# Performance work log

Measured on AMD Instinct MI355X. Metric: run time of the kernel, lower is better.

The kernel has to match this reference:

```python
import math
import jax, jax.numpy as jnp
import numpy as np
from jax.scipy.special import erf

BATCH, SEQ, DIM = 2, 4096, 128
EMA_HEADS, DQK, DV = 16, 64, 256
NUM_BUCKETS, MAX_DIST = 32, 128


def _next_fast_len(n):
    # smallest 5-smooth integer >= n (matches scipy.fftpack.next_fast_len)
    while True:
        m = n
        for p in (2, 3, 5):
            while m % p == 0:
                m //= p
        if m == 1:
            return n
        n += 1


def _laplacian_attn(x):
    mu = math.sqrt(0.5)
    std = math.sqrt(0.25 * math.pi)
    return 0.5 * (1.0 + erf((x - mu) / (std * math.sqrt(2.0))))


def _rel_pos_bias(table, n, scale):
    # causal T5 relative position bias, bucket(q_pos - k_pos)
    pos = jnp.arange(n)
    rel = jnp.maximum(pos[:, None] - pos[None, :], 0)  # [n, n], >= 0
    max_exact = NUM_BUCKETS // 2
    is_small = rel < max_exact
    val_large = max_exact + (
        jnp.log(jnp.maximum(rel, 1).astype(jnp.float32) / max_exact)
        / math.log(MAX_DIST / max_exact) * (NUM_BUCKETS - max_exact)
    ).astype(jnp.int32)
    val_large = jnp.minimum(val_large, NUM_BUCKETS - 1)
    bucket = jnp.where(is_small, rel, val_large)
    return table[bucket, 0] * scale  # [n, n]


def _conv1d_fft(x, K, n):
    # x: [b, n, h, d] (fft over axis 1), K: [n, h] (fft over axis 0)
    fast_len = _next_fast_len(2 * n - 1)
    f_x = jnp.fft.rfft(x, n=fast_len, axis=1)
    f_K = jnp.fft.rfft(K, n=fast_len, axis=0)
    out = jnp.fft.irfft(f_x * jnp.conj(f_K)[None, :, :, None], fast_len, axis=1)
    out = jnp.roll(out, -1, axis=1)
    return out[:, fast_len - n:]  # [b, n, h, d]


def _forward(x, expansion, reduction, alphas, dampen, Wqk, bqk, gamma, beta,
             Wv, bv, rel_table, Wr, br, Wu, bu, Wh, Uh, bh):
    b, n, d = x.shape
    # ---- multi-headed EMA (causal -> unidirectional) via FFT conv ----
    xe = jnp.einsum('bnd,hd->bnhd', x, expansion)
    a = jax.nn.sigmoid(alphas)            # [h]
    dm = jax.nn.sigmoid(dampen)           # [h]
    powers = jnp.arange(n - 1, -1, -1, dtype=x.dtype)  # reversed powers
    K = a * ((1.0 - a) * dm) ** powers[:, None]        # [n, h]
    conv = _conv1d_fft(xe, K, n)
    ema = jnp.einsum('bnhd,hd->bnd', conv, reduction)  # [b, n, d]
    # ---- single-headed attention (chunk_size=-1 -> one chunk), v from x ----
    qk = jax.nn.silu(ema @ Wqk + bqk)     # [b, n, dqk]
    q = qk * gamma[0] + beta[0]
    k = qk * gamma[1] + beta[1]
    v = jax.nn.silu(x @ Wv + bv)          # [b, n, dv]
    scale = 1.0 / n                       # laplacian_attn_fn scaling
    sim = jnp.einsum('bid,bjd->bij', q, k) * scale
    sim = sim + _rel_pos_bias(rel_table, n, DQK ** 0.5)
    attn = _laplacian_attn(sim)
    causal_mask = jnp.triu(jnp.ones((n, n), dtype=bool), 1)
    attn = jnp.where(causal_mask, 0.0, attn)  # laplacian: zero after activation
    attn_out = jnp.einsum('bij,bjd->bid', attn, v)  # [b, n, dv]
    # ---- gating + output ----
    reset_gate = jax.nn.silu(ema @ Wr + br)         # [b, n, dv]
    update_gate = jax.nn.sigmoid(ema @ Wu + bu)     # [b, n, d]
    gated = attn_out * reset_gate
    H = jax.nn.silu(ema @ Wh + gated @ Uh + bh)     # [b, n, d]
    return update_gate * H + (1.0 - update_gate) * x


def setup_inputs() -> dict:
    key = jax.random.key(0)
    ks = jax.random.split(key, 18)
    def rn(i, shape, s=1.0):
        return jax.random.normal(ks[i], shape, dtype=jnp.float32) * s
    return dict(
        x=rn(0, (BATCH, SEQ, DIM)),
        expansion=rn(1, (EMA_HEADS, DIM), 0.2),
        reduction=rn(2, (EMA_HEADS, DIM), 0.2),
        alphas=rn(3, (EMA_HEADS,)),
        dampen=rn(4, (EMA_HEADS,)),
        Wqk=rn(5, (DIM, DQK), 0.05), bqk=rn(6, (DQK,), 0.02),
        gamma=rn(7, (2, DQK), 0.02), beta=jnp.zeros((2, DQK), jnp.float32),
        Wv=rn(8, (DIM, DV), 0.05), bv=rn(9, (DV,), 0.02),
        rel_table=rn(10, (NUM_BUCKETS, 1), 0.02),
        Wr=rn(11, (DIM, DV), 0.05), br=rn(12, (DV,), 0.02),
        Wu=rn(13, (DIM, DIM), 0.05), bu=rn(14, (DIM,), 0.02),
        Wh=rn(15, (DIM, DIM), 0.05), Uh=rn(16, (DV, DIM), 0.05),
        bh=rn(17, (DIM,), 0.02),
    )


def reference(x, expansion, reduction, alphas, dampen, Wqk, bqk, gamma, beta,
              Wv, bv, rel_table, Wr, br, Wu, bu, Wh, Uh, bh):
    return _forward(x, expansion, reduction, alphas, dampen, Wqk, bqk, gamma,
                    beta, Wv, bv, rel_table, Wr, br, Wu, bu, Wh, Uh, bh)
```

## Files before the change

kernel.cpp:

```cpp
#include <hip/hip_runtime.h>
#include <cstdint>
#include <cmath>

#define B_ 2
#define N_ 4096
#define D_ 128
#define H_ 16
#define DQK_ 64
#define DV_ 256

typedef float    f4_t  __attribute__((ext_vector_type(4)));
typedef float    f16f  __attribute__((ext_vector_type(16)));
typedef _Float16 h4_t  __attribute__((ext_vector_type(4)));
typedef _Float16 h8_t  __attribute__((ext_vector_type(8)));

__device__ __forceinline__ float sigmoidf_(float z) { return 1.f/(1.f + expf(-z)); }
__device__ __forceinline__ float siluf_(float z)    { return z/(1.f + expf(-z)); }
__device__ __forceinline__ f16f zero16() {
  f16f z;
#pragma unroll
  for (int i = 0; i < 16; ++i) z[i] = 0.f;
  return z;
}

__global__ void ema_phase1(const float* __restrict__ x, const float* __restrict__ expansion,
                           const float* __restrict__ alphas, const float* __restrict__ dampen,
                           float* __restrict__ F, _Float16* __restrict__ xh) {
  int bid = blockIdx.x;
  int dg = bid & 7, c = (bid >> 3) & 63, b = bid >> 9;
  int h = threadIdx.x & 15, dl = threadIdx.x >> 4;
  int d = dg*16 + dl;
  float a  = sigmoidf_(alphas[h]);
  float dm = sigmoidf_(dampen[h]);
  float q  = (1.f - a)*dm;
  float coef = a * expansion[h*D_ + d];
  __shared__ float xs[64][16];
  {
    int e = threadIdx.x;
    int t = e >> 2, seg = e & 3;
    const float* xp = x + ((size_t)b*N_ + c*64 + t)*D_ + dg*16 + seg*4;
    f4_t v = *(const f4_t*)xp;
    *(f4_t*)&xs[t][seg*4] = v;
    h4_t hv;
#pragma unroll
    for (int j = 0; j < 4; ++j) hv[j] = (_Float16)v[j];
    *(h4_t*)(xh + ((size_t)b*N_ + c*64 + t)*D_ + dg*16 + seg*4) = hv;
  }
  __syncthreads();
  float s = 0.f;
#pragma unroll
  for (int t = 0; t < 64; ++t) s = fmaf(q, s, coef*xs[t][dl]);
  F[(((size_t)b*H_ + h)*D_ + d)*64 + c] = s;
}

__global__ void ema_carry(const float* __restrict__ F, const float* __restrict__ alphas,
                          const float* __restrict__ dampen, float* __restrict__ carry) {
  int wid = blockIdx.x*4 + (threadIdx.x >> 6);
  int lane = threadIdx.x & 63;
  int h = (wid >> 7) & 15;
  float a  = sigmoidf_(alphas[h]);
  float dm = sigmoidf_(dampen[h]);
  float q  = (1.f - a)*dm;
  float qL = q;
#pragma unroll
  for (int i = 0; i < 6; ++i) qL *= qL;
  float A = qL;
  float Bv = F[(size_t)wid*64 + lane];
#pragma unroll
  for (int len = 1; len < 64; len <<= 1) {
    float Ap = __shfl_up(A, len);
    float Bp = __shfl_up(Bv, len);
    if (lane >= len) { Bv = fmaf(A, Bp, Bv); A = A*Ap; }
  }
  float Bprev = __shfl_up(Bv, 1);
  carry[(size_t)wid*64 + lane] = (lane == 0) ? 0.f : Bprev;
}

__global__ void ema_phase2(const float* __restrict__ x, const float* __restrict__ expansion,
                           const float* __restrict__ reduction,
                           const float* __restrict__ alphas, const float* __restrict__ dampen,
                           const float* __restrict__ carry, _Float16* __restrict__ emah) {
  int bid = blockIdx.x;
  int dg = bid & 7, c = (bid >> 3) & 63, b = bid >> 9;
  int h = threadIdx.x & 15, dl = threadIdx.x >> 4;
  int d = dg*16 + dl;
  float a  = sigmoidf_(alphas[h]);
  float dm = sigmoidf_(dampen[h]);
  float q  = (1.f - a)*dm;
  float coef = a * expansion[h*D_ + d];
  float red  = reduction[h*D_ + d];
  __shared__ float xs[64][16];
  {
    int e = threadIdx.x;
    int t = e >> 2, seg = e & 3;
    const float* xp = x + ((size_t)b*N_ + c*64 + t)*D_ + dg*16 + seg*4;
    *(f4_t*)&xs[t][seg*4] = *(const f4_t*)xp;
  }
  __syncthreads();
  float s = carry[(((size_t)b*H_ + h)*D_ + d)*64 + c];
  for (int t = 0; t < 64; ++t) {
    s = fmaf(q, s, coef*xs[t][dl]);
    float v = red * s;
    v += __shfl_xor(v, 1); v += __shfl_xor(v, 2);
    v += __shfl_xor(v, 4); v += __shfl_xor(v, 8);
    if (h == 0) emah[((size_t)b*N_ + c*64 + t)*D_ + d] = (_Float16)v;
  }
}

__global__ void prep_all(const float* __restrict__ Wqk, const float* __restrict__ Wv,
                         const float* __restrict__ Wr, const float* __restrict__ Wu,
                         const float* __restrict__ Wh,
                         const float* __restrict__ bqk, const float* __restrict__ bv,
                         const float* __restrict__ br, const float* __restrict__ bu,
                         const float* __restrict__ bh,
                         const float* __restrict__ Uh, const float* __restrict__ rel_table,
                         _Float16* __restrict__ Wt, float* __restrict__ bcat,
                         _Float16* __restrict__ Uht, float* __restrict__ bias2T) {
  int idx = blockIdx.x*256 + threadIdx.x;
  if (idx < 832*128) {
    int c = idx >> 7, d = idx & 127;
    const float* W; const float* bias; int ncol, cl;
    if (c < 64)       { W=Wqk; bias=bqk; ncol=64;  cl=c; }
    else if (c < 320) { W=Wv;  bias=bv;  ncol=256; cl=c-64; }
    else if (c < 576) { W=Wr;  bias=br;  ncol=256; cl=c-320; }
    else if (c < 704) { W=Wu;  bias=bu;  ncol=128; cl=c-576; }
    else              { W=Wh;  bias=bh;  ncol=128; cl=c-704; }
    Wt[idx] = (_Float16)W[d*ncol + cl];
    if (d == 0) bcat[c] = bias[cl];
  } else if (idx < 832*128 + 32768) {
    int i2 = idx - 832*128;
    int k = i2 >> 7, c = i2 & 127;
    Uht[(size_t)c*256 + k] = (_Float16)Uh[i2];
  } else if (idx < 832*128 + 32768 + 4096) {
    int r = idx - (832*128 + 32768);
    int bucket;
    if (r < 16) bucket = r;
    else {
      double v = log((double)r / 16.0) / log(8.0) * 16.0;
      bucket = 16 + (int)v;
      if (bucket > 31) bucket = 31;
    }
    bias2T[r] = (rel_table[bucket]*8.0f - 0.70710678f) * 1.1283792f;
  }
}

__global__ __launch_bounds__(256) void linear_mfma(
    const _Float16* __restrict__ emah, const _Float16* __restrict__ xh,
    const _Float16* __restrict__ Wt, const float* __restrict__ bcat,
    const float* __restrict__ gamma, const float* __restrict__ beta,
    _Float16* __restrict__ qh, _Float16* __restrict__ kh, _Float16* __restrict__ vTt,
    _Float16* __restrict__ resetbh, _Float16* __restrict__ updatebh,
    float* __restrict__ hemab) {
  int slab = blockIdx.x % 13, rt = blockIdx.x / 13;
  int tid = threadIdx.x;
  int lane = tid & 63, w = tid >> 6;
  int lr = lane & 15, lg = lane >> 4;
  int mode = (slab==0)?0:(slab<5)?1:(slab<9)?2:(slab<11)?3:4;
  const _Float16* src = (mode==1) ? xh : emah;
  __shared__ _Float16 As[64][136];
  __shared__ _Float16 Ws[64][136];
  {
    const h8_t* s8 = (const h8_t*)(src + (size_t)rt*64*D_);
#pragma unroll
    for (int i = 0; i < 4; ++i) {
      int idx = tid + i*256;
      int row = idx >> 4, seg = idx & 15;
      *(h8_t*)&As[row][seg*8] = s8[idx];
    }
    const h8_t* w8 = (const h8_t*)(Wt + (size_t)slab*64*D_);
#pragma unroll
    for (int i = 0; i < 4; ++i) {
      int idx = tid + i*256;
      int row = idx >> 4, seg = idx & 15;
      *(h8_t*)&Ws[row][seg*8] = w8[idx];
    }
  }
  __syncthreads();
  h4_t af[8];
#pragma unroll
  for (int ks = 0; ks < 8; ++ks) af[ks] = *(const h4_t*)&As[w*16 + lr][ks*16 + lg*4];
  int row0 = rt*64 + w*16 + lg*4;
#pragma unroll
  for (int ns = 0; ns < 4; ++ns) {
    f4_t acc = (f4_t){0.f,0.f,0.f,0.f};
#pragma unroll
    for (int ks = 0; ks < 8; ++ks) {
      h4_t bf = *(const h4_t*)&Ws[ns*16 + lr][ks*16 + lg*4];
      acc = __builtin_amdgcn_mfma_f32_16x16x16f16(af[ks], bf, acc, 0, 0, 0);
    }
    int c = slab*64 + ns*16 + lr;
    float bias = bcat[c];
    if (mode == 0) {
      float g0 = gamma[c], g1 = gamma[64+c], be0 = beta[c], be1 = beta[64+c];
#pragma unroll
      for (int r = 0; r < 4; ++r) {
        float qk = siluf_(acc[r] + bias);
        size_t row = row0 + r;
        qh[row*DQK_ + c] = (_Float16)(qk*g0 + be0);
        kh[row*DQK_ + c] = (_Float16)(qk*g1 + be1);
      }
    } else if (mode == 1) {
      int cl = c - 64;
      int bb = row0 >> 12, rl = row0 & 4095;
      h4_t vv;
#pragma unroll
      for (int r = 0; r < 4; ++r) vv[r] = (_Float16)siluf_(acc[r] + bias);
      *(h4_t*)&vTt[(((size_t)bb*128 + (rl>>5))*256 + cl)*32 + (rl&31)] = vv;
    } else if (mode == 2) {
      int cl = c - 320;
#pragma unroll
      for (int r = 0; r < 4; ++r)
        resetbh[(size_t)(row0 + r)*DV_ + cl] = (_Float16)siluf_(acc[r] + bias);
    } else if (mode == 3) {
      int cl = c - 576;
#pragma unroll
      for (int r = 0; r < 4; ++r)
        updatebh[(size_t)(row0 + r)*D_ + cl] = (_Float16)sigmoidf_(acc[r] + bias);
    } else {
      int cl = c - 704;
#pragma unroll
      for (int r = 0; r < 4; ++r) hemab[(size_t)(row0 + r)*D_ + cl] = acc[r] + bias;
    }
  }
}

__global__ __launch_bounds__(512, 2) void attn_kernel(
    const _Float16* __restrict__ qh, const _Float16* __restrict__ kh,
    const _Float16* __restrict__ vTt, const float* __restrict__ bias2T,
    _Float16* __restrict__ attnp) {
  int bid = blockIdx.x;
  int ip = 31 - (bid >> 5);
  int rem = bid & 31;
  int s = rem >> 1, b = rem & 1;
  int nblk = (ip + 2) >> 1;
  if (s >= nblk) return;
  int T = 4*ip + 4;
  int tlo = (s*T)/nblk, thi = ((s+1)*T)/nblk;
  int nt = thi - tlo;
  int tq = ip >> 1;
  int base = (ip & 1) ? (tq+1)*(tq+1) : tq*(tq+1);
  int slot = base + s;
  int i0 = ip*128;
  int tid = threadIdx.x;
  int lane = tid & 63, w = tid >> 6;
  int iq = w & 3;
  int dvh = w >> 2;
  bool prod = (dvh == 0);
  int lm = lane & 31, lg = lane >> 5;

  __shared__ __align__(16) char Vb[2][18432];
  __shared__ __align__(16) char Kb[2][4352];
  __shared__ __align__(16) char Pb[2][4][2560];
  __shared__ float biasW[384];

  int jmaxv = thi*32 - 1;
  int dlo = i0 - jmaxv;
  int cnt = 128 + jmaxv - tlo*32;
  for (int k = tid; k < cnt; k += 512) {
    int d = dlo + k;
    biasW[k] = d < 0 ? -1e38f : bias2T[d];
  }

  h4_t qf[8];
  if (prod) {
    const _Float16* qp = qh + ((size_t)b*N_ + i0 + iq*32 + lm)*DQK_ + 4*lg;
#pragma unroll
    for (int ksq = 0; ksq < 8; ++ksq) qf[ksq] = *(const h4_t*)(qp + 8*ksq);
  }

  f16f accO[4];
#pragma unroll
  for (int i = 0; i < 4; ++i) accO[i] = zero16();

  const _Float16* kbase = kh + (size_t)b*N_*DQK_;
  const _Float16* vbase = vTt + (size_t)b*128*8192;
  int st = tid & 255;
  int kr = st >> 3, kc = st & 7;

  h8_t k8r, vr4[4];
#define ISSUE_(JT) { \
  k8r = *(const h8_t*)(kbase + (size_t)((JT)*32 + kr)*DQK_ + kc*8); \
  const _Float16* vp_ = vbase + (size_t)(JT)*8192 + st*32; \
  _Pragma("unroll") for (int i = 0; i < 4; ++i) vr4[i] = *(const h8_t*)(vp_ + i*8); }

#define COMMIT_(BI) { \
  char* ka_ = Kb[BI] + kr*136 + kc*16; \
  *(h4_t*)ka_       = __builtin_shufflevector(k8r, k8r, 0,1,2,3); \
  *(h4_t*)(ka_ + 8) = __builtin_shufflevector(k8r, k8r, 4,5,6,7); \
  char* va_ = Vb[BI] + st*72; \
  _Pragma("unroll") for (int i = 0; i < 4; ++i) { \
    *(h4_t*)(va_ + i*16)     = __builtin_shufflevector(vr4[i], vr4[i], 0,1,2,3); \
    *(h4_t*)(va_ + i*16 + 8) = __builtin_shufflevector(vr4[i], vr4[i], 4,5,6,7); } }

  if (!prod) {
    ISSUE_(tlo);
    COMMIT_(0);
    if (nt > 1) ISSUE_(tlo + 1);
  }
  __syncthreads();

  const float C1 = 1.1283792f / 4096.f;
  int ibase = i0 + iq*32 + lm;
#pragma unroll 1
  for (int t = 0; t < nt; ++t) {
    h4_t pa[4];
    if (prod) {
      const char* kb = Kb[t & 1];
      __builtin_amdgcn_s_setprio(1);
      f16f accS = zero16();
#pragma unroll
      for (int ksq = 0; ksq < 8; ++ksq) {
        h4_t kf = *(const h4_t*)(kb + lm*136 + 16*ksq + 8*lg);
        accS = __builtin_amdgcn_mfma_f32_32x32x8f16(kf, qf[ksq], accS, 0, 0, 0);
      }
      __builtin_amdgcn_s_setprio(0);
      int idx0 = ibase - dlo - (tlo + t)*32 - 4*lg;
#pragma unroll
      for (int rr = 0; rr < 16; ++rr) {
        float tt = fmaf(accS[rr], C1, biasW[idx0 - 8*(rr>>2) - (rr&3)]);
        float e = tt*fmaf(tt*tt, -0.101797f, -2.304877f);
        float u = exp2f(e);
        float pv = __builtin_amdgcn_rcpf(1.f + u);
        pa[rr>>2][rr&3] = (_Float16)pv;
      }
      char* pp = Pb[t & 1][iq] + lane*40;
#pragma unroll
      for (int k2 = 0; k2 < 4; ++k2) *(h4_t*)(pp + k2*8) = pa[k2];
    } else {
      if (t+1 < nt) COMMIT_((t+1) & 1);
      if (t+2 < nt) ISSUE_(tlo + t + 2);
    }
    __syncthreads();
    if (!prod) {
      const char* pp = Pb[t & 1][iq] + lane*40;
#pragma unroll
      for (int k2 = 0; k2 < 4; ++k2) pa[k2] = *(const h4_t*)(pp + k2*8);
    }
    const char* vb = Vb[t & 1];
    __builtin_amdgcn_s_setprio(1);
#pragma unroll
    for (int ks = 0; ks < 4; ++ks) {
#pragma unroll
      for (int dvb = 0; dvb < 4; ++dvb) {
        h4_t vf = *(const h4_t*)(vb + (dvh*128 + dvb*32 + lm)*72 + 16*ks + 8*lg);
        accO[dvb] = __builtin_amdgcn_mfma_f32_32x32x8f16(pa[ks], vf, accO[dvb], 0, 0, 0);
      }
    }
    __builtin_amdgcn_s_setprio(0);
    __syncthreads();
  }
#undef ISSUE_
#undef COMMIT_

  _Float16* op = attnp + ((size_t)b*272 + slot)*(128*256);
#pragma unroll
  for (int dvb = 0; dvb < 4; ++dvb) {
    int col = dvh*128 + dvb*32 + lm;
#pragma unroll
    for (int rr = 0; rr < 16; ++rr) {
      int row = iq*32 + 8*(rr>>2) + 4*lg + (rr&3);
      op[(size_t)row*256 + col] = (_Float16)accO[dvb][rr];
    }
  }
}

__global__ void combine_gated(const _Float16* __restrict__ attnp,
                              const _Float16* __restrict__ resetbh,
                              _Float16* __restrict__ gatedh) {
  size_t fi = (size_t)blockIdx.x*256 + threadIdx.x;
  int c4 = (int)(fi & 63);
  int rr = (int)(fi >> 6);
  int b = rr >> 12, n = rr & 4095;
  int ip = n >> 7, rowLocal = n & 127;
  int nblk = (ip + 2) >> 1;
  int tq = ip >> 1;
  int base = (ip & 1) ? (tq+1)*(tq+1) : tq*(tq+1);
  const _Float16* ap = attnp + ((size_t)b*272 + base)*32768 + (size_t)rowLocal*256 + c4*4;
  f4_t acc = (f4_t){0.f,0.f,0.f,0.f};
  for (int s2 = 0; s2 < nblk; ++s2) {
    h4_t pv = *(const h4_t*)(ap + (size_t)s2*32768);
#pragma unroll
    for (int j = 0; j < 4; ++j) acc[j] += (float)pv[j];
  }
  h4_t rg = *(const h4_t*)(resetbh + fi*4);
  h4_t hg;
#pragma unroll
  for (int j = 0; j < 4; ++j) hg[j] = (_Float16)(acc[j] * (float)rg[j]);
  *(h4_t*)(gatedh + fi*4) = hg;
}

__global__ __launch_bounds__(256) void final_mfma(
    const _Float16* __restrict__ gatedh, const _Float16* __restrict__ Uht,
    const float* __restrict__ hemab, const _Float16* __restrict__ updatebh,
    const float* __restrict__ x, float* __restrict__ out) {
  int rt = blockIdx.x >> 1, cs = blockIdx.x & 1;
  int tid = threadIdx.x;
  int lane = tid & 63, w = tid >> 6;
  int lr = lane & 15, lg = lane >> 4;
  int row0 = rt*64, c0 = cs*64;
  __shared__ _Float16 As[64][136];
  __shared__ _Float16 Ws[64][136];
  f4_t acc[4];
#pragma unroll
  for (int ns = 0; ns < 4; ++ns) acc[ns] = (f4_t){0.f,0.f,0.f,0.f};
#pragma unroll
  for (int kc = 0; kc < 2; ++kc) {
    __syncthreads();
#pragma unroll
    for (int i = 0; i < 4; ++i) {
      int idx = tid + i*256;
      int row = idx >> 4, seg = idx & 15;
      *(h8_t*)&As[row][seg*8] =
          *(const h8_t*)(gatedh + (size_t)(row0 + row)*DV_ + kc*128 + seg*8);
      *(h8_t*)&Ws[row][seg*8] =
          *(const h8_t*)(Uht + (size_t)(c0 + row)*DV_ + kc*128 + seg*8);
    }
    __syncthreads();
    h4_t af[8];
#pragma unroll
    for (int ks = 0; ks < 8; ++ks) af[ks] = *(const h4_t*)&As[w*16 + lr][ks*16 + lg*4];
#pragma unroll
    for (int ns = 0; ns < 4; ++ns) {
#pragma unroll
      for (int ks = 0; ks < 8; ++ks) {
        h4_t bf = *(const h4_t*)&Ws[ns*16 + lr][ks*16 + lg*4];
        acc[ns] = __builtin_amdgcn_mfma_f32_16x16x16f16(af[ks], bf, acc[ns], 0, 0, 0);
      }
    }
  }
  int orow = row0 + w*16 + lg*4;
#pragma unroll
  for (int ns = 0; ns < 4; ++ns) {
    int col = c0 + ns*16 + lr;
#pragma unroll
    for (int r = 0; r < 4; ++r) {
      size_t o = (size_t)(orow + r)*D_ + col;
      float z = acc[ns][r] + hemab[o];
      float Hv = siluf_(z);
      float u  = (float)updatebh[o];
      out[o] = u*Hv + (1.f - u)*x[o];
    }
  }
}

extern "C" void kernel_launch(void* const* d_in, const int* in_sizes, int n_in,
                              void* d_out, int out_size, void* d_ws, size_t ws_size,
                              hipStream_t stream) {
  (void)in_sizes; (void)n_in; (void)out_size; (void)ws_size;
  const float* x         = (const float*)d_in[0];
  const float* expansion = (const float*)d_in[1];
  const float* reduction = (const float*)d_in[2];
  const float* alphas    = (const float*)d_in[3];
  const float* dampen    = (const float*)d_in[4];
  const float* Wqk       = (const float*)d_in[5];
  const float* bqk       = (const float*)d_in[6];
  const float* gamma     = (const float*)d_in[7];
  const float* beta      = (const float*)d_in[8];
  const float* Wv        = (const float*)d_in[9];
  const float* bv        = (const float*)d_in[10];
  const float* rel_table = (const float*)d_in[11];
  const float* Wr        = (const float*)d_in[12];
  const float* br        = (const float*)d_in[13];
  const float* Wu        = (const float*)d_in[14];
  const float* bu        = (const float*)d_in[15];
  const float* Wh        = (const float*)d_in[16];
  const float* Uh        = (const float*)d_in[17];
  const float* bh        = (const float*)d_in[18];
  float* out = (float*)d_out;

  char* p = (char*)d_ws;
  size_t off = 0;
  auto alloc = [&](size_t bytes) -> char* {
    char* r = p + off;
    off += (bytes + 255) & ~(size_t)255;
    return r;
  };
  float*    F       = (float*)alloc((size_t)B_*H_*D_*64*4);
  float*    carry   = (float*)alloc((size_t)B_*H_*D_*64*4);
  _Float16* emah    = (_Float16*)alloc((size_t)B_*N_*D_*2);
  _Float16* xh      = (_Float16*)alloc((size_t)B_*N_*D_*2);
  float*    bias2T  = (float*)alloc((size_t)N_*4);
  _Float16* Wt      = (_Float16*)alloc((size_t)832*128*2);
  float*    bcat    = (float*)alloc((size_t)832*4);
  _Float16* Uht     = (_Float16*)alloc((size_t)D_*DV_*2);
  _Float16* qh      = (_Float16*)alloc((size_t)B_*N_*DQK_*2);
  _Float16* kh      = (_Float16*)alloc((size_t)B_*N_*DQK_*2);
  _Float16* vTt     = (_Float16*)alloc((size_t)B_*DV_*N_*2);
  _Float16* resetbh = (_Float16*)alloc((size_t)B_*N_*DV_*2);
  _Float16* updatebh= (_Float16*)alloc((size_t)B_*N_*D_*2);
  float*    hemab   = (float*)alloc((size_t)B_*N_*D_*4);
  _Float16* gatedh  = (_Float16*)alloc((size_t)B_*N_*DV_*2);
  _Float16* attnp   = (_Float16*)alloc((size_t)B_*272*128*256*2);

  prep_all<<<560, 256, 0, stream>>>(Wqk, Wv, Wr, Wu, Wh, bqk, bv, br, bu, bh,
                                    Uh, rel_table, Wt, bcat, Uht, bias2T);
  ema_phase1<<<1024, 256, 0, stream>>>(x, expansion, alphas, dampen, F, xh);
  ema_carry<<<1024, 256, 0, stream>>>(F, alphas, dampen, carry);
  ema_phase2<<<1024, 256, 0, stream>>>(x, expansion, reduction, alphas, dampen, carry, emah);
  linear_mfma<<<128*13, 256, 0, stream>>>(emah, xh, Wt, bcat, gamma, beta,
                                          qh, kh, vTt, resetbh, updatebh, hemab);
  attn_kernel<<<1024, 512, 0, stream>>>(qh, kh, vTt, bias2T, attnp);
  combine_gated<<<2048, 256, 0, stream>>>(attnp, resetbh, gatedh);
  final_mfma<<<256, 256, 0, stream>>>(gatedh, Uht, hemab, updatebh, x, out);
}
```

Baseline: 122.5 us.

## Halve attention query tile, load K into registers, and software-pipeline QK ahead of PV

```diff
diff --git a/kernel.cpp b/kernel.cpp
--- a/kernel.cpp
+++ b/kernel.cpp
@@ -224,115 +224,134 @@
   }
 }
 
-__global__ __launch_bounds__(512, 2) void attn_kernel(
+__global__ __launch_bounds__(256, 3) void attn_kernel(
     const _Float16* __restrict__ qh, const _Float16* __restrict__ kh,
     const _Float16* __restrict__ vTt, const float* __restrict__ bias2T,
     _Float16* __restrict__ attnp) {
   int bid = blockIdx.x;
-  int ip = 31 - (bid >> 5);
+  int it = 63 - (bid >> 5);
   int rem = bid & 31;
   int s = rem >> 1, b = rem & 1;
-  int nblk = (ip + 2) >> 1;
+  int a = it >> 2, r = it & 3;
+  int nblk = a + 1;
   if (s >= nblk) return;
-  int T = 4*ip + 4;
+  int T = 2*it + 2;
   int tlo = (s*T)/nblk, thi = ((s+1)*T)/nblk;
   int nt = thi - tlo;
-  int tq = ip >> 1;
-  int base = (ip & 1) ? (tq+1)*(tq+1) : tq*(tq+1);
+  int base = it + 2*a*(a-1) + r*a;
   int slot = base + s;
-  int i0 = ip*128;
+  int i0 = it * 64;
   int tid = threadIdx.x;
   int lane = tid & 63, w = tid >> 6;
-  int iq = w & 3;
-  int dvh = w >> 2;
+  int ih = w & 1;
+  int dvh = w >> 1;
   bool prod = (dvh == 0);
   int lm = lane & 31, lg = lane >> 5;
 
   __shared__ __align__(16) char Vb[2][18432];
-  __shared__ __align__(16) char Kb[2][4352];
-  __shared__ __align__(16) char Pb[2][4][2560];
-  __shared__ float biasW[384];
+  __shared__ __align__(16) char Pb[2][2][2560];
+  __shared__ float biasW[320];
 
   int jmaxv = thi*32 - 1;
   int dlo = i0 - jmaxv;
-  int cnt = 128 + jmaxv - tlo*32;
-  for (int k = tid; k < cnt; k += 512) {
+  int cnt = 64 + jmaxv - tlo*32;
+  for (int k = tid; k < cnt; k += 256) {
     int d = dlo + k;
     biasW[k] = d < 0 ? -1e38f : bias2T[d];
   }
 
-  h4_t qf[8];
-  if (prod) {
-    const _Float16* qp = qh + ((size_t)b*N_ + i0 + iq*32 + lm)*DQK_ + 4*lg;
-#pragma unroll
-    for (int ksq = 0; ksq < 8; ++ksq) qf[ksq] = *(const h4_t*)(qp + 8*ksq);
-  }
-
-  f16f accO[4];
-#pragma unroll
-  for (int i = 0; i < 4; ++i) accO[i] = zero16();
-
   const _Float16* kbase = kh + (size_t)b*N_*DQK_;
   const _Float16* vbase = vTt + (size_t)b*128*8192;
-  int st = tid & 255;
-  int kr = st >> 3, kc = st & 7;
-
-  h8_t k8r, vr4[4];
-#define ISSUE_(JT) { \
-  k8r = *(const h8_t*)(kbase + (size_t)((JT)*32 + kr)*DQK_ + kc*8); \
-  const _Float16* vp_ = vbase + (size_t)(JT)*8192 + st*32; \
-  _Pragma("unroll") for (int i = 0; i < 4; ++i) vr4[i] = *(const h8_t*)(vp_ + i*8); }
-
-#define COMMIT_(BI) { \
-  char* ka_ = Kb[BI] + kr*136 + kc*16; \
-  *(h4_t*)ka_       = __builtin_shufflevector(k8r, k8r, 0,1,2,3); \
-  *(h4_t*)(ka_ + 8) = __builtin_shufflevector(k8r, k8r, 4,5,6,7); \
-  char* va_ = Vb[BI] + st*72; \
+
+  h4_t qf[8], knxt[8];
+  if (prod) {
+    const _Float16* qp = qh + ((size_t)b*N_ + i0 + ih*32 + lm)*DQK_ + 4*lg;
+#pragma unroll
+    for (int ksq = 0; ksq < 8; ++ksq) qf[ksq] = *(const h4_t*)(qp + 8*ksq);
+  }
+
+#define KISSUE_(JT) { \
+  const _Float16* kp_ = kbase + (size_t)((JT)*32 + lm)*DQK_ + 4*lg; \
+  _Pragma("unroll") for (int ksq = 0; ksq < 8; ++ksq) knxt[ksq] = *(const h4_t*)(kp_ + 8*ksq); }
+
+  f16f accO[4];
+#pragma unroll
+  for (int i = 0; i < 4; ++i) accO[i] = zero16();
+
+  int st = tid & 127;
+  h8_t vr[8];
+#define VISSUE_(JT) { \
+  const _Float16* vp_ = vbase + (size_t)(JT)*8192 + st*64; \
+  _Pragma("unroll") for (int i = 0; i < 8; ++i) vr[i] = *(const h8_t*)(vp_ + i*8); }
+
+#define VCOMMIT_(BI) { \
+  char* va_ = Vb[BI] + (2*st)*72; \
   _Pragma("unroll") for (int i = 0; i < 4; ++i) { \
-    *(h4_t*)(va_ + i*16)     = __builtin_shufflevector(vr4[i], vr4[i], 0,1,2,3); \
-    *(h4_t*)(va_ + i*16 + 8) = __builtin_shufflevector(vr4[i], vr4[i], 4,5,6,7); } }
+    *(h4_t*)(va_ + i*16)     = __builtin_shufflevector(vr[i], vr[i], 0,1,2,3); \
+    *(h4_t*)(va_ + i*16 + 8) = __builtin_shufflevector(vr[i], vr[i], 4,5,6,7); } \
+  char* vb2_ = Vb[BI] + (2*st + 1)*72; \
+  _Pragma("unroll") for (int i = 0; i < 4; ++i) { \
+    *(h4_t*)(vb2_ + i*16)     = __builtin_shufflevector(vr[4+i], vr[4+i], 0,1,2,3); \
+    *(h4_t*)(vb2_ + i*16 + 8) = __builtin_shufflevector(vr[4+i], vr[4+i], 4,5,6,7); } }
+
+  const float C1 = 1.1283792f / 4096.f;
+  int ibase = i0 + ih*32 + lm;
+
+#define SOFTMAX_(JT, ACC, PA) { \
+  int idx0 = ibase - dlo - (JT)*32 - 4*lg; \
+  _Pragma("unroll") for (int rr = 0; rr < 16; ++rr) { \
+    float tt = fmaf((ACC)[rr], C1, biasW[idx0 - 8*(rr>>2) - (rr&3)]); \
+    float e = tt*fmaf(tt*tt, -0.101797f, -2.304877f); \
+    float u = exp2f(e); \
+    float pv = __builtin_amdgcn_rcpf(1.f + u); \
+    (PA)[rr>>2][rr&3] = (_Float16)pv; } }
 
   if (!prod) {
-    ISSUE_(tlo);
-    COMMIT_(0);
-    if (nt > 1) ISSUE_(tlo + 1);
+    VISSUE_(tlo);
+    VCOMMIT_(0);
+    if (nt > 1) VISSUE_(tlo + 1);
+  } else {
+    KISSUE_(tlo);
   }
   __syncthreads();
 
-  const float C1 = 1.1283792f / 4096.f;
-  int ibase = i0 + iq*32 + lm;
+  h4_t paP[4];
+  if (prod) {
+    f16f accS = zero16();
+#pragma unroll
+    for (int ksq = 0; ksq < 8; ++ksq)
+      accS = __builtin_amdgcn_mfma_f32_32x32x8f16(knxt[ksq], qf[ksq], accS, 0, 0, 0);
+    if (nt > 1) KISSUE_(tlo + 1);
+    SOFTMAX_(tlo, accS, paP);
+    char* pp = Pb[0][ih] + lane*40;
+#pragma unroll
+    for (int k2 = 0; k2 < 4; ++k2) *(h4_t*)(pp + k2*8) = paP[k2];
+  }
+  __syncthreads();
+
 #pragma unroll 1
   for (int t = 0; t < nt; ++t) {
-    h4_t pa[4];
+    h4_t pa[4], pan[4];
     if (prod) {
-      const char* kb = Kb[t & 1];
-      __builtin_amdgcn_s_setprio(1);
-      f16f accS = zero16();
-#pragma unroll
-      for (int ksq = 0; ksq < 8; ++ksq) {
-        h4_t kf = *(const h4_t*)(kb + lm*136 + 16*ksq + 8*lg);
-        accS = __builtin_amdgcn_mfma_f32_32x32x8f16(kf, qf[ksq], accS, 0, 0, 0);
+      if (t+1 < nt) {
+        __builtin_amdgcn_s_setprio(1);
+        f16f accS = zero16();
+#pragma unroll
+        for (int ksq = 0; ksq < 8; ++ksq)
+          accS = __builtin_amdgcn_mfma_f32_32x32x8f16(knxt[ksq], qf[ksq], accS, 0, 0, 0);
+        __builtin_amdgcn_s_setprio(0);
+        if (t+2 < nt) KISSUE_(tlo + t + 2);
+        SOFTMAX_(tlo + t + 1, accS, pan);
+        char* pp = Pb[(t+1) & 1][ih] + lane*40;
+#pragma unroll
+        for (int k2 = 0; k2 < 4; ++k2) *(h4_t*)(pp + k2*8) = pan[k2];
       }
-      __builtin_amdgcn_s_setprio(0);
-      int idx0 = ibase - dlo - (tlo + t)*32 - 4*lg;
-#pragma unroll
-      for (int rr = 0; rr < 16; ++rr) {
-        float tt = fmaf(accS[rr], C1, biasW[idx0 - 8*(rr>>2) - (rr&3)]);
-        float e = tt*fmaf(tt*tt, -0.101797f, -2.304877f);
-        float u = exp2f(e);
-        float pv = __builtin_amdgcn_rcpf(1.f + u);
-        pa[rr>>2][rr&3] = (_Float16)pv;
-      }
-      char* pp = Pb[t & 1][iq] + lane*40;
-#pragma unroll
-      for (int k2 = 0; k2 < 4; ++k2) *(h4_t*)(pp + k2*8) = pa[k2];
+#pragma unroll
+      for (int k2 = 0; k2 < 4; ++k2) pa[k2] = paP[k2];
     } else {
-      if (t+1 < nt) COMMIT_((t+1) & 1);
-      if (t+2 < nt) ISSUE_(tlo + t + 2);
-    }
-    __syncthreads();
-    if (!prod) {
-      const char* pp = Pb[t & 1][iq] + lane*40;
+      if (t+1 < nt) VCOMMIT_((t+1) & 1);
+      if (t+2 < nt) VISSUE_(tlo + t + 2);
+      const char* pp = Pb[t & 1][ih] + lane*40;
 #pragma unroll
       for (int k2 = 0; k2 < 4; ++k2) pa[k2] = *(const h4_t*)(pp + k2*8);
     }
@@ -348,17 +367,23 @@
     }
     __builtin_amdgcn_s_setprio(0);
     __syncthreads();
-  }
-#undef ISSUE_
-#undef COMMIT_
-
-  _Float16* op = attnp + ((size_t)b*272 + slot)*(128*256);
+    if (prod) {
+#pragma unroll
+      for (int k2 = 0; k2 < 4; ++k2) paP[k2] = pan[k2];
+    }
+  }
+#undef KISSUE_
+#undef VISSUE_
+#undef VCOMMIT_
+#undef SOFTMAX_
+
+  _Float16* op = attnp + ((size_t)b*544 + slot)*(64*256);
 #pragma unroll
   for (int dvb = 0; dvb < 4; ++dvb) {
     int col = dvh*128 + dvb*32 + lm;
 #pragma unroll
     for (int rr = 0; rr < 16; ++rr) {
-      int row = iq*32 + 8*(rr>>2) + 4*lg + (rr&3);
+      int row = ih*32 + 8*(rr>>2) + 4*lg + (rr&3);
       op[(size_t)row*256 + col] = (_Float16)accO[dvb][rr];
     }
   }
@@ -371,14 +396,14 @@
   int c4 = (int)(fi & 63);
   int rr = (int)(fi >> 6);
   int b = rr >> 12, n = rr & 4095;
-  int ip = n >> 7, rowLocal = n & 127;
-  int nblk = (ip + 2) >> 1;
-  int tq = ip >> 1;
-  int base = (ip & 1) ? (tq+1)*(tq+1) : tq*(tq+1);
-  const _Float16* ap = attnp + ((size_t)b*272 + base)*32768 + (size_t)rowLocal*256 + c4*4;
+  int it = n >> 6, rowLocal = n & 63;
+  int a = it >> 2, r = it & 3;
+  int nblk = a + 1;
+  int base = it + 2*a*(a-1) + r*a;
+  const _Float16* ap = attnp + ((size_t)b*544 + base)*16384 + rowLocal*256 + c4*4;
   f4_t acc = (f4_t){0.f,0.f,0.f,0.f};
   for (int s2 = 0; s2 < nblk; ++s2) {
-    h4_t pv = *(const h4_t*)(ap + (size_t)s2*32768);
+    h4_t pv = *(const h4_t*)(ap + (size_t)s2*16384);
 #pragma unroll
     for (int j = 0; j < 4; ++j) acc[j] += (float)pv[j];
   }
@@ -490,7 +515,7 @@
   _Float16* updatebh= (_Float16*)alloc((size_t)B_*N_*D_*2);
   float*    hemab   = (float*)alloc((size_t)B_*N_*D_*4);
   _Float16* gatedh  = (_Float16*)alloc((size_t)B_*N_*DV_*2);
-  _Float16* attnp   = (_Float16*)alloc((size_t)B_*272*128*256*2);
+  _Float16* attnp   = (_Float16*)alloc((size_t)B_*544*64*256*2);
 
   prep_all<<<560, 256, 0, stream>>>(Wqk, Wv, Wr, Wu, Wh, bqk, bv, br, bu, bh,
                                     Uh, rel_table, Wt, bcat, Uht, bias2T);
@@ -499,7 +524,7 @@
   ema_phase2<<<1024, 256, 0, stream>>>(x, expansion, reduction, alphas, dampen, carry, emah);
   linear_mfma<<<128*13, 256, 0, stream>>>(emah, xh, Wt, bcat, gamma, beta,
                                           qh, kh, vTt, resetbh, updatebh, hemab);
-  attn_kernel<<<1024, 512, 0, stream>>>(qh, kh, vTt, bias2T, attnp);
+  attn_kernel<<<2048, 256, 0, stream>>>(qh, kh, vTt, bias2T, attnp);
   combine_gated<<<2048, 256, 0, stream>>>(attnp, resetbh, gatedh);
   final_mfma<<<256, 256, 0, stream>>>(gatedh, Uht, hemab, updatebh, x, out);
 }
```

Result: slower. 167.4 us (+36.7%).

## Restructure attention to independent per-wave 32-row tiles without shared memory

Applied to the files above, without the earlier changes.

```diff
diff --git a/kernel.cpp b/kernel.cpp
--- a/kernel.cpp
+++ b/kernel.cpp
@@ -224,141 +224,99 @@
   }
 }
 
-__global__ __launch_bounds__(512, 2) void attn_kernel(
+__global__ __launch_bounds__(256, 2) void attn_kernel(
     const _Float16* __restrict__ qh, const _Float16* __restrict__ kh,
     const _Float16* __restrict__ vTt, const float* __restrict__ bias2T,
     _Float16* __restrict__ attnp) {
   int bid = blockIdx.x;
-  int ip = 31 - (bid >> 5);
-  int rem = bid & 31;
-  int s = rem >> 1, b = rem & 1;
-  int nblk = (ip + 2) >> 1;
+  int i32 = 127 - (bid >> 3);
+  int rem = bid & 7;
+  int b = rem & 1, sg = rem >> 1;
+  int w = threadIdx.x >> 6, lane = threadIdx.x & 63;
+  int s = sg*4 + w;
+  int nblk = (i32 >> 3) + 1;
   if (s >= nblk) return;
-  int T = 4*ip + 4;
+  int T = i32 + 1;
   int tlo = (s*T)/nblk, thi = ((s+1)*T)/nblk;
   int nt = thi - tlo;
-  int tq = ip >> 1;
-  int base = (ip & 1) ? (tq+1)*(tq+1) : tq*(tq+1);
+  int t8 = i32 >> 3, r8 = i32 & 7;
+  int base = i32 + 4*t8*(t8-1) + r8*t8;
   int slot = base + s;
-  int i0 = ip*128;
-  int tid = threadIdx.x;
-  int lane = tid & 63, w = tid >> 6;
-  int iq = w & 3;
-  int dvh = w >> 2;
-  bool prod = (dvh == 0);
+  int i0 = i32*32;
   int lm = lane & 31, lg = lane >> 5;
-
-  __shared__ __align__(16) char Vb[2][18432];
-  __shared__ __align__(16) char Kb[2][4352];
-  __shared__ __align__(16) char Pb[2][4][2560];
-  __shared__ float biasW[384];
-
-  int jmaxv = thi*32 - 1;
-  int dlo = i0 - jmaxv;
-  int cnt = 128 + jmaxv - tlo*32;
-  for (int k = tid; k < cnt; k += 512) {
-    int d = dlo + k;
-    biasW[k] = d < 0 ? -1e38f : bias2T[d];
-  }
-
-  h4_t qf[8];
-  if (prod) {
-    const _Float16* qp = qh + ((size_t)b*N_ + i0 + iq*32 + lm)*DQK_ + 4*lg;
-#pragma unroll
-    for (int ksq = 0; ksq < 8; ++ksq) qf[ksq] = *(const h4_t*)(qp + 8*ksq);
-  }
-
-  f16f accO[4];
-#pragma unroll
-  for (int i = 0; i < 4; ++i) accO[i] = zero16();
 
   const _Float16* kbase = kh + (size_t)b*N_*DQK_;
   const _Float16* vbase = vTt + (size_t)b*128*8192;
-  int st = tid & 255;
-  int kr = st >> 3, kc = st & 7;
-
-  h8_t k8r, vr4[4];
-#define ISSUE_(JT) { \
-  k8r = *(const h8_t*)(kbase + (size_t)((JT)*32 + kr)*DQK_ + kc*8); \
-  const _Float16* vp_ = vbase + (size_t)(JT)*8192 + st*32; \
-  _Pragma("unroll") for (int i = 0; i < 4; ++i) vr4[i] = *(const h8_t*)(vp_ + i*8); }
-
-#define COMMIT_(BI) { \
-  char* ka_ = Kb[BI] + kr*136 + kc*16; \
-  *(h4_t*)ka_       = __builtin_shufflevector(k8r, k8r, 0,1,2,3); \
-  *(h4_t*)(ka_ + 8) = __builtin_shufflevector(k8r, k8r, 4,5,6,7); \
-  char* va_ = Vb[BI] + st*72; \
-  _Pragma("unroll") for (int i = 0; i < 4; ++i) { \
-    *(h4_t*)(va_ + i*16)     = __builtin_shufflevector(vr4[i], vr4[i], 0,1,2,3); \
-    *(h4_t*)(va_ + i*16 + 8) = __builtin_shufflevector(vr4[i], vr4[i], 4,5,6,7); } }
-
-  if (!prod) {
-    ISSUE_(tlo);
-    COMMIT_(0);
-    if (nt > 1) ISSUE_(tlo + 1);
-  }
-  __syncthreads();
+
+  h4_t qf[8];
+  {
+    const _Float16* qp = qh + ((size_t)b*N_ + i0 + lm)*DQK_ + 4*lg;
+#pragma unroll
+    for (int ksq = 0; ksq < 8; ++ksq) qf[ksq] = *(const h4_t*)(qp + 8*ksq);
+  }
+
+  f16f accO[8];
+#pragma unroll
+  for (int i = 0; i < 8; ++i) accO[i] = zero16();
+
+  h4_t kn[8];
+#define KISSUE_(JT) { \
+  const _Float16* kp_ = kbase + (size_t)((JT)*32 + lm)*DQK_ + 4*lg; \
+  _Pragma("unroll") for (int ksq = 0; ksq < 8; ++ksq) kn[ksq] = *(const h4_t*)(kp_ + 8*ksq); }
+
+  KISSUE_(tlo);
 
   const float C1 = 1.1283792f / 4096.f;
-  int ibase = i0 + iq*32 + lm;
+  int ibase = i0 + lm;
 #pragma unroll 1
   for (int t = 0; t < nt; ++t) {
+    int j0 = (tlo + t)*32;
+    const _Float16* vt = vbase + (size_t)(tlo + t)*8192;
+    f16f accS = zero16();
+#pragma unroll
+    for (int ksq = 0; ksq < 8; ++ksq)
+      accS = __builtin_amdgcn_mfma_f32_32x32x8f16(kn[ksq], qf[ksq], accS, 0, 0, 0);
+    if (t+1 < nt) KISSUE_(tlo + t + 1);
     h4_t pa[4];
-    if (prod) {
-      const char* kb = Kb[t & 1];
-      __builtin_amdgcn_s_setprio(1);
-      f16f accS = zero16();
-#pragma unroll
-      for (int ksq = 0; ksq < 8; ++ksq) {
-        h4_t kf = *(const h4_t*)(kb + lm*136 + 16*ksq + 8*lg);
-        accS = __builtin_amdgcn_mfma_f32_32x32x8f16(kf, qf[ksq], accS, 0, 0, 0);
+#pragma unroll
+    for (int rr = 0; rr < 16; ++rr) {
+      int j = j0 + 8*(rr>>2) + (rr&3) + 4*lg;
+      int d = ibase - j;
+      float bb = (d < 0) ? -1e38f : bias2T[d < 0 ? 0 : d];
+      float tt = fmaf(accS[rr], C1, bb);
+      float e = tt*fmaf(tt*tt, -0.101797f, -2.304877f);
+      float u = exp2f(e);
+      float pv = __builtin_amdgcn_rcpf(1.f + u);
+      pa[rr>>2][rr&3] = (_Float16)pv;
+    }
+    h4_t vA[4], vB[4];
+#pragma unroll
+    for (int ks = 0; ks < 4; ++ks) vA[ks] = *(const h4_t*)(vt + lm*32 + ks*8 + 4*lg);
+    __builtin_amdgcn_s_setprio(1);
+#pragma unroll
+    for (int dvb = 0; dvb < 8; ++dvb) {
+      h4_t* cur = (dvb & 1) ? vB : vA;
+      h4_t* nxt = (dvb & 1) ? vA : vB;
+      if (dvb < 7) {
+        const _Float16* vp = vt + ((dvb+1)*32 + lm)*32 + 4*lg;
+#pragma unroll
+        for (int ks = 0; ks < 4; ++ks) nxt[ks] = *(const h4_t*)(vp + ks*8);
       }
-      __builtin_amdgcn_s_setprio(0);
-      int idx0 = ibase - dlo - (tlo + t)*32 - 4*lg;
-#pragma unroll
-      for (int rr = 0; rr < 16; ++rr) {
-        float tt = fmaf(accS[rr], C1, biasW[idx0 - 8*(rr>>2) - (rr&3)]);
-        float e = tt*fmaf(tt*tt, -0.101797f, -2.304877f);
-        float u = exp2f(e);
-        float pv = __builtin_amdgcn_rcpf(1.f + u);
-        pa[rr>>2][rr&3] = (_Float16)pv;
-      }
-      char* pp = Pb[t & 1][iq] + lane*40;
-#pragma unroll
-      for (int k2 = 0; k2 < 4; ++k2) *(h4_t*)(pp + k2*8) = pa[k2];
-    } else {
-      if (t+1 < nt) COMMIT_((t+1) & 1);
-      if (t+2 < nt) ISSUE_(tlo + t + 2);
-    }
-    __syncthreads();
-    if (!prod) {
-      const char* pp = Pb[t & 1][iq] + lane*40;
-#pragma unroll
-      for (int k2 = 0; k2 < 4; ++k2) pa[k2] = *(const h4_t*)(pp + k2*8);
-    }
-    const char* vb = Vb[t & 1];
-    __builtin_amdgcn_s_setprio(1);
-#pragma unroll
-    for (int ks = 0; ks < 4; ++ks) {
-#pragma unroll
-      for (int dvb = 0; dvb < 4; ++dvb) {
-        h4_t vf = *(const h4_t*)(vb + (dvh*128 + dvb*32 + lm)*72 + 16*ks + 8*lg);
-        accO[dvb] = __builtin_amdgcn_mfma_f32_32x32x8f16(pa[ks], vf, accO[dvb], 0, 0, 0);
-      }
+#pragma unroll
+      for (int ks = 0; ks < 4; ++ks)
+        accO[dvb] = __builtin_amdgcn_mfma_f32_32x32x8f16(pa[ks], cur[ks], accO[dvb], 0, 0, 0);
     }
     __builtin_amdgcn_s_setprio(0);
-    __syncthreads();
-  }
-#undef ISSUE_
-#undef COMMIT_
-
-  _Float16* op = attnp + ((size_t)b*272 + slot)*(128*256);
-#pragma unroll
-  for (int dvb = 0; dvb < 4; ++dvb) {
-    int col = dvh*128 + dvb*32 + lm;
+  }
+#undef KISSUE_
+
+  _Float16* op = attnp + ((size_t)b*1088 + slot)*(32*256);
+#pragma unroll
+  for (int dvb = 0; dvb < 8; ++dvb) {
+    int col = dvb*32 + lm;
 #pragma unroll
     for (int rr = 0; rr < 16; ++rr) {
-      int row = iq*32 + 8*(rr>>2) + 4*lg + (rr&3);
+      int row = 8*(rr>>2) + 4*lg + (rr&3);
       op[(size_t)row*256 + col] = (_Float16)accO[dvb][rr];
     }
   }
@@ -371,14 +329,14 @@
   int c4 = (int)(fi & 63);
   int rr = (int)(fi >> 6);
   int b = rr >> 12, n = rr & 4095;
-  int ip = n >> 7, rowLocal = n & 127;
-  int nblk = (ip + 2) >> 1;
-  int tq = ip >> 1;
-  int base = (ip & 1) ? (tq+1)*(tq+1) : tq*(tq+1);
-  const _Float16* ap = attnp + ((size_t)b*272 + base)*32768 + (size_t)rowLocal*256 + c4*4;
+  int i32 = n >> 5, rowLocal = n & 31;
+  int nblk = (i32 >> 3) + 1;
+  int t8 = i32 >> 3, r8 = i32 & 7;
+  int base = i32 + 4*t8*(t8-1) + r8*t8;
+  const _Float16* ap = attnp + ((size_t)b*1088 + base)*8192 + (size_t)rowLocal*256 + c4*4;
   f4_t acc = (f4_t){0.f,0.f,0.f,0.f};
   for (int s2 = 0; s2 < nblk; ++s2) {
-    h4_t pv = *(const h4_t*)(ap + (size_t)s2*32768);
+    h4_t pv = *(const h4_t*)(ap + (size_t)s2*8192);
 #pragma unroll
     for (int j = 0; j < 4; ++j) acc[j] += (float)pv[j];
   }
@@ -490,7 +448,7 @@
   _Float16* updatebh= (_Float16*)alloc((size_t)B_*N_*D_*2);
   float*    hemab   = (float*)alloc((size_t)B_*N_*D_*4);
   _Float16* gatedh  = (_Float16*)alloc((size_t)B_*N_*DV_*2);
-  _Float16* attnp   = (_Float16*)alloc((size_t)B_*272*128*256*2);
+  _Float16* attnp   = (_Float16*)alloc((size_t)B_*1088*32*256*2);
 
   prep_all<<<560, 256, 0, stream>>>(Wqk, Wv, Wr, Wu, Wh, bqk, bv, br, bu, bh,
                                     Uh, rel_table, Wt, bcat, Uht, bias2T);
@@ -499,7 +457,7 @@
   ema_phase2<<<1024, 256, 0, stream>>>(x, expansion, reduction, alphas, dampen, carry, emah);
   linear_mfma<<<128*13, 256, 0, stream>>>(emah, xh, Wt, bcat, gamma, beta,
                                           qh, kh, vTt, resetbh, updatebh, hemab);
-  attn_kernel<<<1024, 512, 0, stream>>>(qh, kh, vTt, bias2T, attnp);
+  attn_kernel<<<1024, 256, 0, stream>>>(qh, kh, vTt, bias2T, attnp);
   combine_gated<<<2048, 256, 0, stream>>>(attnp, resetbh, gatedh);
   final_mfma<<<256, 256, 0, stream>>>(gatedh, Uht, hemab, updatebh, x, out);
 }
```

Result: slower. 160.5 us (+31.0%).
